# Kernel tuning notes

Hardware: AMD Instinct MI355X
Metric: run time of the kernel (lower is better)

## Reference

```python
import jax, jax.numpy as jnp
import numpy as np

BN_EPS = 1e-5

def binarize(v):
    # sign binarization with straight-through estimator (grad clipped to |v|<=1),
    # matching the Binarize autograd function used by BinarizeConv2d.
    c = jnp.clip(v, -1.0, 1.0)
    return c + jax.lax.stop_gradient(jnp.sign(v) - c)

def setup_inputs() -> dict:
    key = jax.random.key(0)
    kx, kw = jax.random.split(key)
    x = jax.random.normal(kx, (32, 64, 112, 112), dtype=jnp.float32)
    W = jax.random.normal(kw, (64, 64, 3, 3), dtype=jnp.float32) * 0.05
    gamma = jnp.ones((64,), dtype=jnp.float32)
    beta = jnp.zeros((64,), dtype=jnp.float32)
    return {"x": x, "W": W, "gamma": gamma, "beta": beta}

def reference(x, W, gamma, beta):
    residual = x
    # binet-style scaled binary conv: sign(x) * sign(W) conv, scaled per output
    # channel by alpha = mean(|W|) over (in, kh, kw)
    xb = binarize(x)
    wb = binarize(W)
    alpha = jnp.mean(jnp.abs(W), axis=(1, 2, 3))  # [Cout]
    out = jax.lax.conv_general_dilated(
        xb, wb,
        window_strides=(1, 1), padding=((1, 1), (1, 1)),
        dimension_numbers=("NCHW", "OIHW", "NCHW"))
    out = out * alpha[None, :, None, None]
    # BatchNorm2d (training mode: batch statistics over N,H,W)
    mu = jnp.mean(out, axis=(0, 2, 3), keepdims=True)
    var = jnp.var(out, axis=(0, 2, 3), keepdims=True)
    out = (out - mu) * jax.lax.rsqrt(var + BN_EPS)
    out = out * gamma[None, :, None, None] + beta[None, :, None, None]
    # Hardtanh
    out = jnp.clip(out, -1.0, 1.0)
    # residual add (downsample=None, stride=1)
    return out + residual
```

## Files before the change

### kernel.cpp

```cpp
#include <hip/hip_runtime.h>
#include <cstdint>

typedef unsigned long long u64;

#define HW    12544
#define NCH   64
#define NBATCH 32
#define NPIX  401408

__global__ __launch_bounds__(256) void k_pack(const float* __restrict__ x,
                                              const float* __restrict__ Wt,
                                              u64* __restrict__ xbits,
                                              u64* __restrict__ wbits,
                                              float* __restrict__ alpha) {
  int b = blockIdx.x;
  int t = threadIdx.x;
  if (b < 1568) {
    int n = b / 49;
    int p = (b % 49) * 256 + t;
    const float* xp = x + (size_t)n * NCH * HW + p;
    u64 m = 0;
#pragma unroll 16
    for (int c = 0; c < 64; ++c) {
      m |= (u64)(xp[(size_t)c * HW] > 0.0f) << c;
    }
    xbits[(size_t)n * HW + p] = m;
  } else {
    int wv = t >> 6, lane = t & 63;
    for (int i = 0; i < 16; ++i) {
      int co = wv * 16 + i;
      const float* wp = Wt + ((size_t)co * 64 + lane) * 9;
      float w9[9];
      float s = 0.0f;
#pragma unroll
      for (int k = 0; k < 9; ++k) { w9[k] = wp[k]; s += fabsf(w9[k]); }
#pragma unroll
      for (int off = 32; off > 0; off >>= 1) s += __shfl_xor(s, off);
#pragma unroll
      for (int k = 0; k < 9; ++k) {
        u64 msk = __ballot(w9[k] > 0.0f);
        if (lane == 0) wbits[k * 64 + co] = msk;
      }
      if (lane == 0) alpha[co] = s * (1.0f / 576.0f);
    }
  }
}

__global__ __launch_bounds__(256) void k_stats(const u64* __restrict__ xbits,
                                               const u64* __restrict__ wbits,
                                               u64* __restrict__ S1,
                                               u64* __restrict__ S2) {
  __shared__ u64 stg[4][114];
  __shared__ int corr[9][64];
  __shared__ int red1[256];
  __shared__ int red2[256];
  int b = blockIdx.x, t = threadIdx.x;
  int n = b / 56, h0 = (b % 56) * 2;

  for (int i = t; i < 4 * 114; i += 256) {
    int r = i / 114, cc = i % 114;
    int h = h0 - 1 + r, w = cc - 1;
    u64 v = 0;
    if (h >= 0 && h < 112 && (unsigned)w < 112u)
      v = xbits[(size_t)n * HW + h * 112 + w];
    stg[r][cc] = v;
  }

  int c = t & 63, wv = t >> 6;
  u64 wm[9];
#pragma unroll
  for (int k = 0; k < 9; ++k) wm[k] = wbits[k * 64 + c];

  if (t < 64) {
    int pw[9];
#pragma unroll
    for (int k = 0; k < 9; ++k) pw[k] = __popcll(wm[k]);
#pragma unroll
    for (int ht = 0; ht < 3; ++ht)
#pragma unroll
      for (int wt = 0; wt < 3; ++wt) {
        int s = 0;
#pragma unroll
        for (int k = 0; k < 9; ++k) {
          int dh = k / 3 - 1, dw = k % 3 - 1;
          bool inval = (ht == 0 && dh < 0) || (ht == 2 && dh > 0) ||
                       (wt == 0 && dw < 0) || (wt == 2 && dw > 0);
          if (inval) s += 64 - 2 * pw[k];
        }
        corr[ht * 3 + wt][t] = s;
      }
  }
  __syncthreads();

  int s1 = 0, s2 = 0;
  for (int k = 0; k < 56; ++k) {
    int pl = wv * 56 + k;
    int hl = pl / 112, w = pl % 112;
    int h = h0 + hl;
    int ht = (h == 0) ? 0 : ((h == 111) ? 2 : 1);
    int wt = (w == 0) ? 0 : ((w == 111) ? 2 : 1);
    int sum = 0;
#pragma unroll
    for (int kk = 0; kk < 9; ++kk)
      sum += __popcll(stg[hl + kk / 3][w + kk % 3] ^ wm[kk]);
    int I = 576 - 2 * sum - corr[ht * 3 + wt][c];
    s1 += I;
    s2 += I * I;
  }
  red1[t] = s1; red2[t] = s2;
  __syncthreads();
  if (t < 64) {
    int a1 = red1[t] + red1[t + 64] + red1[t + 128] + red1[t + 192];
    int a2 = red2[t] + red2[t + 64] + red2[t + 128] + red2[t + 192];
    atomicAdd(&S1[t], (u64)(long long)a1);
    atomicAdd(&S2[t], (u64)(long long)a2);
  }
}

__global__ __launch_bounds__(256) void k_final(const float* __restrict__ x,
                                               const u64* __restrict__ xbits,
                                               const u64* __restrict__ wbits,
                                               const u64* __restrict__ S1,
                                               const u64* __restrict__ S2,
                                               const float* __restrict__ alpha,
                                               const float* __restrict__ gamma,
                                               const float* __restrict__ beta,
                                               float* __restrict__ out) {
  __shared__ u64 stg[4][114];
  __shared__ u64 wsh[576];
  __shared__ int corr[9][64];
  __shared__ float scs[64];
  __shared__ float bis[64];
  int b = blockIdx.x, t = threadIdx.x;
  int n = b / 56, h0 = (b % 56) * 2;

  for (int i = t; i < 4 * 114; i += 256) {
    int r = i / 114, cc = i % 114;
    int h = h0 - 1 + r, w = cc - 1;
    u64 v = 0;
    if (h >= 0 && h < 112 && (unsigned)w < 112u)
      v = xbits[(size_t)n * HW + h * 112 + w];
    stg[r][cc] = v;
  }
  for (int i = t; i < 576; i += 256) wsh[i] = wbits[i];

  if (t < 64) {
    int pw[9];
#pragma unroll
    for (int k = 0; k < 9; ++k) pw[k] = __popcll(wbits[k * 64 + t]);
#pragma unroll
    for (int ht = 0; ht < 3; ++ht)
#pragma unroll
      for (int wt = 0; wt < 3; ++wt) {
        int s = 0;
#pragma unroll
        for (int k = 0; k < 9; ++k) {
          int dh = k / 3 - 1, dw = k % 3 - 1;
          bool inval = (ht == 0 && dh < 0) || (ht == 2 && dh > 0) ||
                       (wt == 0 && dw < 0) || (wt == 2 && dw > 0);
          if (inval) s += 64 - 2 * pw[k];
        }
        corr[ht * 3 + wt][t] = s;
      }
    long long s1 = (long long)S1[t];
    long long s2 = (long long)S2[t];
    double inv = 1.0 / (double)NPIX;
    double mean = (double)s1 * inv;
    double var = (double)s2 * inv - mean * mean;
    double al = (double)alpha[t];
    double rs = 1.0 / sqrt(al * al * var + 1e-5);
    double sc = (double)gamma[t] * al * rs;
    scs[t] = (float)sc;
    bis[t] = (float)((double)beta[t] - sc * mean);
  }
  __syncthreads();

  if (t < 224) {
    int hl = t / 112, w = t % 112;
    int h = h0 + hl;
    int ht = (h == 0) ? 0 : ((h == 111) ? 2 : 1);
    int wt = (w == 0) ? 0 : ((w == 111) ? 2 : 1);
    int type = ht * 3 + wt;
    u64 xm[9];
#pragma unroll
    for (int kk = 0; kk < 9; ++kk) xm[kk] = stg[hl + kk / 3][w + kk % 3];
    const float* xp = x + (size_t)n * NCH * HW + (size_t)h * 112 + w;
    float* op = out + (size_t)n * NCH * HW + (size_t)h * 112 + w;
#pragma unroll 4
    for (int c = 0; c < 64; ++c) {
      int sum = 0;
#pragma unroll
      for (int kk = 0; kk < 9; ++kk) sum += __popcll(xm[kk] ^ wsh[kk * 64 + c]);
      int I = 576 - 2 * sum - corr[type][c];
      float o = fmaf((float)I, scs[c], bis[c]);
      o = fminf(fmaxf(o, -1.0f), 1.0f);
      op[(size_t)c * HW] = o + xp[(size_t)c * HW];
    }
  }
}

extern "C" void kernel_launch(void* const* d_in, const int* in_sizes, int n_in,
                              void* d_out, int out_size, void* d_ws, size_t ws_size,
                              hipStream_t stream) {
  const float* x     = (const float*)d_in[0];
  const float* W     = (const float*)d_in[1];
  const float* gamma = (const float*)d_in[2];
  const float* beta  = (const float*)d_in[3];
  float* out = (float*)d_out;

  char* ws = (char*)d_ws;
  u64*  S1    = (u64*)(ws + 0);
  u64*  S2    = (u64*)(ws + 512);
  float* alpha = (float*)(ws + 1024);
  u64*  wbits = (u64*)(ws + 2048);
  u64*  xbits = (u64*)(ws + 8192);

  hipMemsetAsync(ws, 0, 1024, stream);

  hipLaunchKernelGGL(k_pack, dim3(1569), dim3(256), 0, stream, x, W, xbits, wbits, alpha);
  hipLaunchKernelGGL(k_stats, dim3(32 * 56), dim3(256), 0, stream, xbits, wbits, S1, S2);
  hipLaunchKernelGGL(k_final, dim3(32 * 56), dim3(256), 0, stream,
                     x, xbits, wbits, S1, S2, alpha, gamma, beta, out);
}
```

Before: 276.6 us.

## Fuse pack, stats and final passes into one cooperative persistent kernel

Replaces the three launches and memset with a single cooperative kernel of 448 blocks, each owning an 8-row strip. The strip's sign bits are packed straight into shared memory with float4 loads, so the global xbits buffer goes away. Two grid syncs separate weight packing, statistics accumulation and the final output. Each thread now computes four adjacent pixels so the halo bit words can be reused, and BN bias and boundary corrections are folded into per-type float tables. The cost is grid-wide barriers and low occupancy: one block per strip at 256 threads, with a 256,2 launch bound.

```diff
diff --git a/kernel.cpp b/kernel.cpp
--- a/kernel.cpp
+++ b/kernel.cpp
@@ -1,200 +1,200 @@
 #include <hip/hip_runtime.h>
+#include <hip/hip_cooperative_groups.h>
 #include <cstdint>
 
+namespace cg = cooperative_groups;
 typedef unsigned long long u64;
 
-#define HW    12544
-#define NCH   64
-#define NBATCH 32
-#define NPIX  401408
-
-__global__ __launch_bounds__(256) void k_pack(const float* __restrict__ x,
-                                              const float* __restrict__ Wt,
-                                              u64* __restrict__ xbits,
-                                              u64* __restrict__ wbits,
-                                              float* __restrict__ alpha) {
-  int b = blockIdx.x;
-  int t = threadIdx.x;
-  if (b < 1568) {
-    int n = b / 49;
-    int p = (b % 49) * 256 + t;
-    const float* xp = x + (size_t)n * NCH * HW + p;
-    u64 m = 0;
-#pragma unroll 16
+#define HW   12544
+#define NPIX 401408
+
+__global__ __launch_bounds__(256, 2) void k_fused(
+    const float* __restrict__ x, const float* __restrict__ Wt,
+    const float* __restrict__ gamma, const float* __restrict__ beta,
+    float* __restrict__ out,
+    u64* __restrict__ S1, u64* __restrict__ S2,
+    float* __restrict__ alpha9, u64* __restrict__ wbits) {
+  __shared__ u64 stg[10][114];
+  __shared__ int red1[256];
+  __shared__ int red2[256];
+  __shared__ float mscS[64];
+  __shared__ float b3S[9][64];
+  cg::grid_group grid = cg::this_grid();
+  int b = blockIdx.x, t = threadIdx.x;
+  int n = b / 14, h0 = (b % 14) * 8;
+
+  {
+    u64* stg1 = &stg[0][0];
+    for (int i = t; i < 1140; i += 256) stg1[i] = 0;
+  }
+  __syncthreads();
+  {
+    int rlo = (h0 == 0) ? 1 : 0;
+    int rhi = (h0 == 104) ? 8 : 9;
+    int P = (rhi - rlo + 1) * 112;
+    const float* base = x + (size_t)(n * 64) * HW + (h0 - 1 + rlo) * 112;
+    u64 m0x = 0, m0y = 0, m0z = 0, m0w = 0;
+    u64 m1x = 0, m1y = 0, m1z = 0, m1w = 0;
+    int p0 = 4 * t, p1 = 1024 + 4 * t;
+    bool a0 = p0 < P, a1 = p1 < P;
     for (int c = 0; c < 64; ++c) {
-      m |= (u64)(xp[(size_t)c * HW] > 0.0f) << c;
-    }
-    xbits[(size_t)n * HW + p] = m;
-  } else {
-    int wv = t >> 6, lane = t & 63;
+      const float* cb = base + (size_t)c * HW;
+      if (a0) {
+        float4 v = *reinterpret_cast<const float4*>(cb + p0);
+        m0x |= (u64)(v.x > 0.f) << c; m0y |= (u64)(v.y > 0.f) << c;
+        m0z |= (u64)(v.z > 0.f) << c; m0w |= (u64)(v.w > 0.f) << c;
+      }
+      if (a1) {
+        float4 v = *reinterpret_cast<const float4*>(cb + p1);
+        m1x |= (u64)(v.x > 0.f) << c; m1y |= (u64)(v.y > 0.f) << c;
+        m1z |= (u64)(v.z > 0.f) << c; m1w |= (u64)(v.w > 0.f) << c;
+      }
+    }
+    if (a0) { int r = rlo + p0 / 112, col = p0 % 112;
+      stg[r][col+1] = m0x; stg[r][col+2] = m0y; stg[r][col+3] = m0z; stg[r][col+4] = m0w; }
+    if (a1) { int r = rlo + p1 / 112, col = p1 % 112;
+      stg[r][col+1] = m1x; stg[r][col+2] = m1y; stg[r][col+3] = m1z; stg[r][col+4] = m1w; }
+  }
+  if (b < 9) {
+    int lane = t & 63, wv = t >> 6;
     for (int i = 0; i < 16; ++i) {
       int co = wv * 16 + i;
-      const float* wp = Wt + ((size_t)co * 64 + lane) * 9;
-      float w9[9];
-      float s = 0.0f;
-#pragma unroll
-      for (int k = 0; k < 9; ++k) { w9[k] = wp[k]; s += fabsf(w9[k]); }
+      float v = Wt[((size_t)co * 64 + lane) * 9 + b];
+      float s = fabsf(v);
 #pragma unroll
       for (int off = 32; off > 0; off >>= 1) s += __shfl_xor(s, off);
-#pragma unroll
-      for (int k = 0; k < 9; ++k) {
-        u64 msk = __ballot(w9[k] > 0.0f);
-        if (lane == 0) wbits[k * 64 + co] = msk;
-      }
-      if (lane == 0) alpha[co] = s * (1.0f / 576.0f);
-    }
-  }
-}
-
-__global__ __launch_bounds__(256) void k_stats(const u64* __restrict__ xbits,
-                                               const u64* __restrict__ wbits,
-                                               u64* __restrict__ S1,
-                                               u64* __restrict__ S2) {
-  __shared__ u64 stg[4][114];
-  __shared__ int corr[9][64];
-  __shared__ int red1[256];
-  __shared__ int red2[256];
-  int b = blockIdx.x, t = threadIdx.x;
-  int n = b / 56, h0 = (b % 56) * 2;
-
-  for (int i = t; i < 4 * 114; i += 256) {
-    int r = i / 114, cc = i % 114;
-    int h = h0 - 1 + r, w = cc - 1;
-    u64 v = 0;
-    if (h >= 0 && h < 112 && (unsigned)w < 112u)
-      v = xbits[(size_t)n * HW + h * 112 + w];
-    stg[r][cc] = v;
-  }
-
-  int c = t & 63, wv = t >> 6;
-  u64 wm[9];
-#pragma unroll
-  for (int k = 0; k < 9; ++k) wm[k] = wbits[k * 64 + c];
+      u64 msk = __ballot(v > 0.f);
+      if (lane == 0) { wbits[b * 64 + co] = msk; alpha9[b * 64 + co] = s; }
+    }
+  } else if (b == 9) {
+    if (t < 64) S1[t] = 0; else if (t < 128) S2[t - 64] = 0;
+  }
+
+  grid.sync();
+
+  {
+    int c = t & 63, wv = t >> 6;
+    u64 wm0 = wbits[c],       wm1 = wbits[64 + c],  wm2 = wbits[128 + c];
+    u64 wm3 = wbits[192 + c], wm4 = wbits[256 + c], wm5 = wbits[320 + c];
+    u64 wm6 = wbits[384 + c], wm7 = wbits[448 + c], wm8 = wbits[512 + c];
+    int pw0 = __popcll(wm0), pw1 = __popcll(wm1), pw2 = __popcll(wm2);
+    int pw3 = __popcll(wm3), pw5 = __popcll(wm5);
+    int pw6 = __popcll(wm6), pw7 = __popcll(wm7), pw8 = __popcll(wm8);
+    int vtop = 192 - 2 * (pw0 + pw1 + pw2);
+    int vbot = 192 - 2 * (pw6 + pw7 + pw8);
+    int hlft = 192 - 2 * (pw0 + pw3 + pw6);
+    int hrgt = 192 - 2 * (pw2 + pw5 + pw8);
+    int cTL = 64 - 2 * pw0, cTR = 64 - 2 * pw2, cBL = 64 - 2 * pw6, cBR = 64 - 2 * pw8;
+    int s1 = 0, s2 = 0;
+    for (int it = 0; it < 56; ++it) {
+      int idx = wv * 56 + it;
+      int r = idx / 28, w0i = (idx % 28) * 4;
+      int h = h0 + r;
+      u64 A0 = stg[r][w0i],   A1 = stg[r][w0i+1], A2 = stg[r][w0i+2];
+      u64 A3 = stg[r][w0i+3], A4 = stg[r][w0i+4], A5 = stg[r][w0i+5];
+      u64 B0 = stg[r+1][w0i],   B1 = stg[r+1][w0i+1], B2 = stg[r+1][w0i+2];
+      u64 B3 = stg[r+1][w0i+3], B4 = stg[r+1][w0i+4], B5 = stg[r+1][w0i+5];
+      u64 C0 = stg[r+2][w0i],   C1 = stg[r+2][w0i+1], C2 = stg[r+2][w0i+2];
+      u64 C3 = stg[r+2][w0i+3], C4 = stg[r+2][w0i+4], C5 = stg[r+2][w0i+5];
+      int rt = (h == 0) ? vtop : ((h == 111) ? vbot : 0);
+      int lc = hlft - ((h == 0) ? cTL : 0) - ((h == 111) ? cBL : 0);
+      int rc = hrgt - ((h == 0) ? cTR : 0) - ((h == 111) ? cBR : 0);
+      int corr0 = rt + ((w0i == 0) ? lc : 0);
+      int corr3 = rt + ((w0i == 108) ? rc : 0);
+#define SUM9(a0,a1,a2,b0,b1,b2,c0,c1,c2)                                     \
+      (__popcll((a0)^wm0)+__popcll((a1)^wm1)+__popcll((a2)^wm2)              \
+      +__popcll((b0)^wm3)+__popcll((b1)^wm4)+__popcll((b2)^wm5)              \
+      +__popcll((c0)^wm6)+__popcll((c1)^wm7)+__popcll((c2)^wm8))
+      int I0 = 576 - 2 * SUM9(A0,A1,A2,B0,B1,B2,C0,C1,C2) - corr0;
+      int I1 = 576 - 2 * SUM9(A1,A2,A3,B1,B2,B3,C1,C2,C3) - rt;
+      int I2 = 576 - 2 * SUM9(A2,A3,A4,B2,B3,B4,C2,C3,C4) - rt;
+      int I3 = 576 - 2 * SUM9(A3,A4,A5,B3,B4,B5,C3,C4,C5) - corr3;
+#undef SUM9
+      s1 += I0 + I1 + I2 + I3;
+      s2 += I0*I0 + I1*I1 + I2*I2 + I3*I3;
+    }
+    red1[t] = s1; red2[t] = s2;
+    __syncthreads();
+    if (t < 64) {
+      int a1s = red1[t] + red1[t+64] + red1[t+128] + red1[t+192];
+      int a2s = red2[t] + red2[t+64] + red2[t+128] + red2[t+192];
+      atomicAdd(&S1[t], (u64)(long long)a1s);
+      atomicAdd(&S2[t], (u64)(long long)a2s);
+    }
+  }
+
+  grid.sync();
 
   if (t < 64) {
-    int pw[9];
-#pragma unroll
-    for (int k = 0; k < 9; ++k) pw[k] = __popcll(wm[k]);
+    int pw[9]; float asum = 0.f;
+#pragma unroll
+    for (int k = 0; k < 9; ++k) {
+      pw[k] = __popcll(wbits[k * 64 + t]);
+      asum += alpha9[k * 64 + t];
+    }
+    double al = (double)asum * (1.0 / 576.0);
+    long long s1v = (long long)S1[t], s2v = (long long)S2[t];
+    double inv = 1.0 / (double)NPIX;
+    double mean = (double)s1v * inv;
+    double var = (double)s2v * inv - mean * mean;
+    double sc = (double)gamma[t] * al / sqrt(al * al * var + 1e-5);
+    double bi = (double)beta[t] - sc * mean;
+    mscS[t] = (float)(-2.0 * sc);
 #pragma unroll
     for (int ht = 0; ht < 3; ++ht)
 #pragma unroll
       for (int wt = 0; wt < 3; ++wt) {
-        int s = 0;
+        int corr = 0;
 #pragma unroll
         for (int k = 0; k < 9; ++k) {
           int dh = k / 3 - 1, dw = k % 3 - 1;
           bool inval = (ht == 0 && dh < 0) || (ht == 2 && dh > 0) ||
                        (wt == 0 && dw < 0) || (wt == 2 && dw > 0);
-          if (inval) s += 64 - 2 * pw[k];
+          if (inval) corr += 64 - 2 * pw[k];
         }
-        corr[ht * 3 + wt][t] = s;
+        b3S[ht * 3 + wt][t] = (float)((576.0 - corr) * sc + bi);
       }
   }
   __syncthreads();
 
-  int s1 = 0, s2 = 0;
-  for (int k = 0; k < 56; ++k) {
-    int pl = wv * 56 + k;
-    int hl = pl / 112, w = pl % 112;
-    int h = h0 + hl;
-    int ht = (h == 0) ? 0 : ((h == 111) ? 2 : 1);
-    int wt = (w == 0) ? 0 : ((w == 111) ? 2 : 1);
-    int sum = 0;
-#pragma unroll
-    for (int kk = 0; kk < 9; ++kk)
-      sum += __popcll(stg[hl + kk / 3][w + kk % 3] ^ wm[kk]);
-    int I = 576 - 2 * sum - corr[ht * 3 + wt][c];
-    s1 += I;
-    s2 += I * I;
-  }
-  red1[t] = s1; red2[t] = s2;
-  __syncthreads();
-  if (t < 64) {
-    int a1 = red1[t] + red1[t + 64] + red1[t + 128] + red1[t + 192];
-    int a2 = red2[t] + red2[t + 64] + red2[t + 128] + red2[t + 192];
-    atomicAdd(&S1[t], (u64)(long long)a1);
-    atomicAdd(&S2[t], (u64)(long long)a2);
-  }
-}
-
-__global__ __launch_bounds__(256) void k_final(const float* __restrict__ x,
-                                               const u64* __restrict__ xbits,
-                                               const u64* __restrict__ wbits,
-                                               const u64* __restrict__ S1,
-                                               const u64* __restrict__ S2,
-                                               const float* __restrict__ alpha,
-                                               const float* __restrict__ gamma,
-                                               const float* __restrict__ beta,
-                                               float* __restrict__ out) {
-  __shared__ u64 stg[4][114];
-  __shared__ u64 wsh[576];
-  __shared__ int corr[9][64];
-  __shared__ float scs[64];
-  __shared__ float bis[64];
-  int b = blockIdx.x, t = threadIdx.x;
-  int n = b / 56, h0 = (b % 56) * 2;
-
-  for (int i = t; i < 4 * 114; i += 256) {
-    int r = i / 114, cc = i % 114;
-    int h = h0 - 1 + r, w = cc - 1;
-    u64 v = 0;
-    if (h >= 0 && h < 112 && (unsigned)w < 112u)
-      v = xbits[(size_t)n * HW + h * 112 + w];
-    stg[r][cc] = v;
-  }
-  for (int i = t; i < 576; i += 256) wsh[i] = wbits[i];
-
-  if (t < 64) {
-    int pw[9];
-#pragma unroll
-    for (int k = 0; k < 9; ++k) pw[k] = __popcll(wbits[k * 64 + t]);
-#pragma unroll
-    for (int ht = 0; ht < 3; ++ht)
-#pragma unroll
-      for (int wt = 0; wt < 3; ++wt) {
-        int s = 0;
-#pragma unroll
-        for (int k = 0; k < 9; ++k) {
-          int dh = k / 3 - 1, dw = k % 3 - 1;
-          bool inval = (ht == 0 && dh < 0) || (ht == 2 && dh > 0) ||
-                       (wt == 0 && dw < 0) || (wt == 2 && dw > 0);
-          if (inval) s += 64 - 2 * pw[k];
-        }
-        corr[ht * 3 + wt][t] = s;
-      }
-    long long s1 = (long long)S1[t];
-    long long s2 = (long long)S2[t];
-    double inv = 1.0 / (double)NPIX;
-    double mean = (double)s1 * inv;
-    double var = (double)s2 * inv - mean * mean;
-    double al = (double)alpha[t];
-    double rs = 1.0 / sqrt(al * al * var + 1e-5);
-    double sc = (double)gamma[t] * al * rs;
-    scs[t] = (float)sc;
-    bis[t] = (float)((double)beta[t] - sc * mean);
-  }
-  __syncthreads();
-
   if (t < 224) {
-    int hl = t / 112, w = t % 112;
-    int h = h0 + hl;
-    int ht = (h == 0) ? 0 : ((h == 111) ? 2 : 1);
-    int wt = (w == 0) ? 0 : ((w == 111) ? 2 : 1);
-    int type = ht * 3 + wt;
-    u64 xm[9];
-#pragma unroll
-    for (int kk = 0; kk < 9; ++kk) xm[kk] = stg[hl + kk / 3][w + kk % 3];
-    const float* xp = x + (size_t)n * NCH * HW + (size_t)h * 112 + w;
-    float* op = out + (size_t)n * NCH * HW + (size_t)h * 112 + w;
-#pragma unroll 4
-    for (int c = 0; c < 64; ++c) {
-      int sum = 0;
-#pragma unroll
-      for (int kk = 0; kk < 9; ++kk) sum += __popcll(xm[kk] ^ wsh[kk * 64 + c]);
-      int I = 576 - 2 * sum - corr[type][c];
-      float o = fmaf((float)I, scs[c], bis[c]);
-      o = fminf(fmaxf(o, -1.0f), 1.0f);
-      op[(size_t)c * HW] = o + xp[(size_t)c * HW];
+    int r = t / 28, w0i = (t % 28) * 4;
+    int h = h0 + r;
+    u64 A0 = stg[r][w0i],   A1 = stg[r][w0i+1], A2 = stg[r][w0i+2];
+    u64 A3 = stg[r][w0i+3], A4 = stg[r][w0i+4], A5 = stg[r][w0i+5];
+    u64 B0 = stg[r+1][w0i],   B1 = stg[r+1][w0i+1], B2 = stg[r+1][w0i+2];
+    u64 B3 = stg[r+1][w0i+3], B4 = stg[r+1][w0i+4], B5 = stg[r+1][w0i+5];
+    u64 C0 = stg[r+2][w0i],   C1 = stg[r+2][w0i+1], C2 = stg[r+2][w0i+2];
+    u64 C3 = stg[r+2][w0i+3], C4 = stg[r+2][w0i+4], C5 = stg[r+2][w0i+5];
+    int row_t = (h == 0) ? 0 : ((h == 111) ? 2 : 1);
+    bool wl = (w0i == 0), wr = (w0i == 108);
+    int tm = row_t * 3 + 1;
+    const float* xb = x + (size_t)(n * 64) * HW + h * 112 + w0i;
+    float* ob = out + (size_t)(n * 64) * HW + h * 112 + w0i;
+#pragma unroll 2
+    for (int cc = 0; cc < 64; ++cc) {
+      u64 w0 = wbits[cc],       w1 = wbits[64 + cc],  w2 = wbits[128 + cc];
+      u64 w3 = wbits[192 + cc], w4 = wbits[256 + cc], w5 = wbits[320 + cc];
+      u64 w6 = wbits[384 + cc], w7 = wbits[448 + cc], w8 = wbits[512 + cc];
+#define SUM9(a0,a1,a2,b0,b1,b2,c0,c1,c2)                                     \
+      (__popcll((a0)^w0)+__popcll((a1)^w1)+__popcll((a2)^w2)                 \
+      +__popcll((b0)^w3)+__popcll((b1)^w4)+__popcll((b2)^w5)                 \
+      +__popcll((c0)^w6)+__popcll((c1)^w7)+__popcll((c2)^w8))
+      int s0 = SUM9(A0,A1,A2,B0,B1,B2,C0,C1,C2);
+      int s1 = SUM9(A1,A2,A3,B1,B2,B3,C1,C2,C3);
+      int s2 = SUM9(A2,A3,A4,B2,B3,B4,C2,C3,C4);
+      int s3 = SUM9(A3,A4,A5,B3,B4,B5,C3,C4,C5);
+#undef SUM9
+      float msc = mscS[cc];
+      float bmid = b3S[tm][cc];
+      float bj0 = wl ? b3S[row_t * 3][cc] : bmid;
+      float bj3 = wr ? b3S[row_t * 3 + 2][cc] : bmid;
+      float4 xv = *reinterpret_cast<const float4*>(xb + (size_t)cc * HW);
+      float o0 = fminf(fmaxf(fmaf((float)s0, msc, bj0),  -1.f), 1.f) + xv.x;
+      float o1 = fminf(fmaxf(fmaf((float)s1, msc, bmid), -1.f), 1.f) + xv.y;
+      float o2 = fminf(fmaxf(fmaf((float)s2, msc, bmid), -1.f), 1.f) + xv.z;
+      float o3 = fminf(fmaxf(fmaf((float)s3, msc, bj3),  -1.f), 1.f) + xv.w;
+      *reinterpret_cast<float4*>(ob + (size_t)cc * HW) = make_float4(o0, o1, o2, o3);
     }
   }
 }
@@ -209,16 +209,13 @@
   float* out = (float*)d_out;
 
   char* ws = (char*)d_ws;
-  u64*  S1    = (u64*)(ws + 0);
-  u64*  S2    = (u64*)(ws + 512);
-  float* alpha = (float*)(ws + 1024);
-  u64*  wbits = (u64*)(ws + 2048);
-  u64*  xbits = (u64*)(ws + 8192);
-
-  hipMemsetAsync(ws, 0, 1024, stream);
-
-  hipLaunchKernelGGL(k_pack, dim3(1569), dim3(256), 0, stream, x, W, xbits, wbits, alpha);
-  hipLaunchKernelGGL(k_stats, dim3(32 * 56), dim3(256), 0, stream, xbits, wbits, S1, S2);
-  hipLaunchKernelGGL(k_final, dim3(32 * 56), dim3(256), 0, stream,
-                     x, xbits, wbits, S1, S2, alpha, gamma, beta, out);
+  u64*   S1     = (u64*)(ws + 0);
+  u64*   S2     = (u64*)(ws + 512);
+  float* alpha9 = (float*)(ws + 1024);
+  u64*   wbits  = (u64*)(ws + 4096);
+
+  void* args[] = {(void*)&x, (void*)&W, (void*)&gamma, (void*)&beta, (void*)&out,
+                  (void*)&S1, (void*)&S2, (void*)&alpha9, (void*)&wbits};
+  hipLaunchCooperativeKernel((const void*)k_fused, dim3(448), dim3(256),
+                             args, 0, stream);
 }
```

Measured after the change: 380.7 us. 1.38x slower.
